# Kernel optimization log

Hardware: AMD Instinct MI355X
Metric: run time of the kernel (lower is better)

Reference implementation:

```python
import jax, jax.numpy as jnp
import numpy as np

N_NODES = 50000
N_EDGES = 600000
IN_F, HID, OUT_F = 602, 128, 41


def _gconv(x, W, b, src, dst, n):
    # DGL GraphConv, norm='both': D_dst^{-1/2} A (D_src^{-1/2} x W) + b
    ones = jnp.ones(src.shape, dtype=x.dtype)
    deg_out = jnp.clip(jax.ops.segment_sum(ones, src, num_segments=n), 1.0)
    deg_in = jnp.clip(jax.ops.segment_sum(ones, dst, num_segments=n), 1.0)
    h = x * jax.lax.rsqrt(deg_out)[:, None]
    h = h @ W  # dense transform first (in_feats > out_feats path)
    agg = jax.ops.segment_sum(h[src], dst, num_segments=n)  # [N, out]
    return agg * jax.lax.rsqrt(deg_in)[:, None] + b


def setup_inputs() -> dict:
    key = jax.random.key(0)
    ks = jax.random.split(key, 8)
    features = jax.random.normal(ks[0], (N_NODES, IN_F), dtype=jnp.float32)
    src = jax.random.randint(ks[1], (N_EDGES,), 0, N_NODES, dtype=jnp.int32)
    dst = jax.random.randint(ks[2], (N_EDGES,), 0, N_NODES, dtype=jnp.int32)
    def glorot(k, fan_in, fan_out):
        s = jnp.sqrt(6.0 / (fan_in + fan_out)).astype(jnp.float32)
        return jax.random.uniform(k, (fan_in, fan_out), jnp.float32, -s, s)
    return {
        'features': features, 'src': src, 'dst': dst,
        'W1': glorot(ks[3], IN_F, HID), 'b1': jnp.zeros((HID,), jnp.float32),
        'W2': glorot(ks[4], HID, HID), 'b2': jnp.zeros((HID,), jnp.float32),
        'W3': glorot(ks[5], HID, HID), 'b3': jnp.zeros((HID,), jnp.float32),
        'Wfc': glorot(ks[6], HID, OUT_F), 'bfc': jnp.zeros((OUT_F,), jnp.float32),
    }


def reference(features, src, dst, W1, b1, W2, b2, W3, b3, Wfc, bfc):
    n = features.shape[0]
    relu = jax.nn.relu
    x = relu(_gconv(features, W1, b1, src, dst, n))  # x = _x
    _x = relu(_gconv(x, W2, b2, src, dst, n))        # branch (layer2)
    x = relu(_gconv(x, W2, b2, src, dst, n))         # main (same layer2)
    x = relu(_gconv(x, W3, b3, src, dst, n))         # layer3
    x = relu(x + _x)                                  # residual + relu
    return x @ Wfc + bfc
```

## Files before the change

### kernel.cpp

```cpp
#include <hip/hip_runtime.h>
#include <hip/hip_bf16.h>

#define NN   50000
#define NE   600000
#define INF  602
#define HID  128
#define OUTF 41
#define NBLK 196

typedef __attribute__((ext_vector_type(8))) short bf16x8;
typedef __attribute__((ext_vector_type(4))) float f32x4;

__device__ inline unsigned short f2bf(float x) {
    unsigned u = __float_as_uint(x);
    unsigned r = u + 0x7FFF + ((u >> 16) & 1);
    return (unsigned short)(r >> 16);
}

#define GLL16(gp, lp) \
    __builtin_amdgcn_global_load_lds((const __attribute__((address_space(1))) unsigned int*)(gp), \
                                     (__attribute__((address_space(3))) unsigned int*)(lp), 16, 0, 0)

__global__ __launch_bounds__(256) void deg_hist_k(const int* __restrict__ src,
                                                  const int* __restrict__ dst,
                                                  int* __restrict__ cnt_out,
                                                  int* __restrict__ cnt_in, int E) {
    int e = blockIdx.x * 256 + threadIdx.x;
    if (e < E) {
        atomicAdd(&cnt_out[src[e]], 1);
        atomicAdd(&cnt_in[dst[e]], 1);
    }
}

__global__ __launch_bounds__(256) void scan1_k(const int* __restrict__ cnt,
                                               int* __restrict__ rowptr,
                                               int* __restrict__ blockSum) {
    __shared__ int tmp[256];
    int tid = threadIdx.x;
    int i = blockIdx.x * 256 + tid;
    int v = (i < NN) ? cnt[i] : 0;
    tmp[tid] = v;
    __syncthreads();
#pragma unroll
    for (int off = 1; off < 256; off <<= 1) {
        int t = (tid >= off) ? tmp[tid - off] : 0;
        __syncthreads();
        tmp[tid] += t;
        __syncthreads();
    }
    if (i < NN) rowptr[i] = tmp[tid] - v;
    if (tid == 255) blockSum[blockIdx.x] = tmp[255];
}

__global__ __launch_bounds__(256) void scan2_k(const int* __restrict__ blockSum,
                                               int* __restrict__ blockOff,
                                               int* __restrict__ rowptr) {
    __shared__ int tmp[256];
    int tid = threadIdx.x;
    int v = (tid < NBLK) ? blockSum[tid] : 0;
    tmp[tid] = v;
    __syncthreads();
#pragma unroll
    for (int off = 1; off < 256; off <<= 1) {
        int t = (tid >= off) ? tmp[tid - off] : 0;
        __syncthreads();
        tmp[tid] += t;
        __syncthreads();
    }
    if (tid < NBLK) blockOff[tid] = tmp[tid] - v;
    if (tid == 255) rowptr[NN] = tmp[255];
}

__global__ __launch_bounds__(256) void scan3_k(int* __restrict__ rowptr,
                                               const int* __restrict__ blockOff,
                                               int* __restrict__ wcur,
                                               const int* __restrict__ cnt_out,
                                               const int* __restrict__ cnt_in,
                                               float* __restrict__ rs_out,
                                               float* __restrict__ rs_in) {
    int i = blockIdx.x * 256 + threadIdx.x;
    if (i < NN) {
        int r = rowptr[i] + blockOff[blockIdx.x];
        rowptr[i] = r;
        wcur[i] = r;
        int co = cnt_out[i]; if (co < 1) co = 1;
        int ci = cnt_in[i];  if (ci < 1) ci = 1;
        rs_out[i] = rsqrtf((float)co);
        rs_in[i]  = rsqrtf((float)ci);
    }
}

__global__ __launch_bounds__(256) void fill_csr_k(const int* __restrict__ src,
                                                  const int* __restrict__ dst,
                                                  int* __restrict__ wcur,
                                                  int* __restrict__ csrsrc, int E) {
    int e = blockIdx.x * 256 + threadIdx.x;
    if (e < E) {
        int p = atomicAdd(&wcur[dst[e]], 1);
        csrsrc[p] = src[e];
    }
}

__device__ inline void prep_w_body(const float* __restrict__ W, int K,
                                   unsigned short* __restrict__ out, int total4, int i) {
    if (i >= total4) return;
    int col = i & 127;
    int k4 = (i >> 7) << 2;
    short4 h;
    h.x = (short)f2bf((k4 + 0 < K) ? W[(size_t)(k4 + 0) * HID + col] : 0.f);
    h.y = (short)f2bf((k4 + 1 < K) ? W[(size_t)(k4 + 1) * HID + col] : 0.f);
    h.z = (short)f2bf((k4 + 2 < K) ? W[(size_t)(k4 + 2) * HID + col] : 0.f);
    h.w = (short)f2bf((k4 + 3 < K) ? W[(size_t)(k4 + 3) * HID + col] : 0.f);
    *(short4*)&out[(size_t)(k4 >> 3) * 1024 + col * 8 + (k4 & 7)] = h;
}

__global__ __launch_bounds__(256) void prep_w_k(const float* __restrict__ W, int K,
                                                unsigned short* __restrict__ out, int total4) {
    prep_w_body(W, K, out, total4, blockIdx.x * 256 + threadIdx.x);
}

__global__ __launch_bounds__(256) void prep_w2_k(const float* __restrict__ Wa,
                                                 unsigned short* __restrict__ outa,
                                                 const float* __restrict__ Wb,
                                                 unsigned short* __restrict__ outb) {
    if (blockIdx.x < 16)
        prep_w_body(Wa, HID, outa, 4096, blockIdx.x * 256 + threadIdx.x);
    else
        prep_w_body(Wb, HID, outb, 4096, (blockIdx.x - 16) * 256 + threadIdx.x);
}

__global__ __launch_bounds__(256) void gemm1_k(const float* __restrict__ A,
                                               const unsigned short* __restrict__ Wt,
                                               const float* __restrict__ rs_out,
                                               unsigned short* __restrict__ H, int n) {
    __shared__ __attribute__((aligned(16))) short As[64 * 136];
    __shared__ __attribute__((aligned(16))) short Bs[16 * 1024];

    const int tid = threadIdx.x;
    const int wave = tid >> 6;
    const int lane = tid & 63;
    const int quad = lane >> 4;
    const int l16 = lane & 15;
    const int rowBase = blockIdx.x * 64;
    const int tileBase = rowBase + wave * 16;

    float4 apf[8];
    auto loadA = [&](int ch) {
        int kb = ch * 128;
#pragma unroll
        for (int c = 0; c < 8; ++c) {
            int f = c * 256 + tid;
            int row = f >> 5;
            int kc = (f & 31) << 2;
            int grow = rowBase + row;
            int gk = kb + kc;
            float4 v = {0.f, 0.f, 0.f, 0.f};
            if (grow < n) {
                if (gk + 3 < INF) {
                    v = *(const float4*)(A + (size_t)grow * INF + gk);
                } else {
                    if (gk + 0 < INF) v.x = A[(size_t)grow * INF + gk + 0];
                    if (gk + 1 < INF) v.y = A[(size_t)grow * INF + gk + 1];
                    if (gk + 2 < INF) v.z = A[(size_t)grow * INF + gk + 2];
                }
            }
            apf[c] = v;
        }
    };
    auto storeA = [&]() {
#pragma unroll
        for (int c = 0; c < 8; ++c) {
            int f = c * 256 + tid;
            int row = f >> 5;
            int kc = (f & 31) << 2;
            short4 h;
            h.x = (short)f2bf(apf[c].x); h.y = (short)f2bf(apf[c].y);
            h.z = (short)f2bf(apf[c].z); h.w = (short)f2bf(apf[c].w);
            *(short4*)&As[row * 136 + kc] = h;
        }
    };
    auto issueB = [&](int ch) {
#pragma unroll
        for (int c = 0; c < 8; ++c)
            GLL16(Wt + (size_t)ch * 16384 + c * 2048 + tid * 8, &Bs[c * 2048 + tid * 8]);
    };

    f32x4 acc[8];
#pragma unroll
    for (int j = 0; j < 8; ++j) acc[j] = (f32x4){0.f, 0.f, 0.f, 0.f};

    loadA(0);
    for (int ch = 0; ch < 5; ++ch) {
        __syncthreads();
        issueB(ch);
        storeA();
        __syncthreads();
        if (ch + 1 < 5) loadA(ch + 1);
#pragma unroll
        for (int s = 0; s < 4; ++s) {
            bf16x8 af = *(const bf16x8*)&As[(wave * 16 + l16) * 136 + s * 32 + quad * 8];
            const short* bg = &Bs[(s * 4 + quad) * 1024 + l16 * 8];
#pragma unroll
            for (int nt = 0; nt < 8; ++nt) {
                bf16x8 bf = *(const bf16x8*)(bg + nt * 128);
                acc[nt] = __builtin_amdgcn_mfma_f32_16x16x32_bf16(af, bf, acc[nt], 0, 0, 0);
            }
        }
    }

#pragma unroll
    for (int r = 0; r < 4; ++r) {
        int row = tileBase + quad * 4 + r;
        if (row < n) {
            float ro = rs_out[row];
#pragma unroll
            for (int nt = 0; nt < 8; ++nt)
                H[(size_t)row * HID + nt * 16 + l16] = f2bf(acc[nt][r] * ro);
        }
    }
}

__global__ __launch_bounds__(256) void gemm_hid_k(const unsigned short* __restrict__ A,
                                                  const unsigned short* __restrict__ Wt,
                                                  unsigned short* __restrict__ H, int n) {
    __shared__ __attribute__((aligned(16))) short As[64 * 136];
    __shared__ __attribute__((aligned(16))) short Bs[16384];

    const int tid = threadIdx.x;
    const int wave = tid >> 6;
    const int lane = tid & 63;
    const int quad = lane >> 4;
    const int l16 = lane & 15;
    const int wm = wave >> 1;
    const int wn = wave & 1;
    const int rowBase = blockIdx.x * 64;

#pragma unroll
    for (int c = 0; c < 8; ++c)
        GLL16(Wt + c * 2048 + tid * 8, &Bs[c * 2048 + tid * 8]);

#pragma unroll
    for (int c = 0; c < 4; ++c) {
        int f = c * 256 + tid;
        int row = f >> 4;
        int k16 = (f & 15) << 3;
        int grow = rowBase + row;
        int4 v = {0, 0, 0, 0};
        if (grow < n) v = *(const int4*)(A + (size_t)grow * HID + k16);
        *(int4*)&As[row * 136 + k16] = v;
    }
    __syncthreads();

    f32x4 acc[2][4];
#pragma unroll
    for (int i = 0; i < 2; ++i)
#pragma unroll
        for (int j = 0; j < 4; ++j) acc[i][j] = (f32x4){0.f, 0.f, 0.f, 0.f};

#pragma unroll
    for (int kq = 0; kq < 4; ++kq) {
        bf16x8 af[2], bfr[4];
#pragma unroll
        for (int mt = 0; mt < 2; ++mt)
            af[mt] = *(const bf16x8*)&As[(wm * 32 + mt * 16 + l16) * 136 + kq * 32 + quad * 8];
#pragma unroll
        for (int nt = 0; nt < 4; ++nt)
            bfr[nt] = *(const bf16x8*)&Bs[(kq * 4 + quad) * 1024 + (wn * 64 + nt * 16 + l16) * 8];
#pragma unroll
        for (int mt = 0; mt < 2; ++mt)
#pragma unroll
            for (int nt = 0; nt < 4; ++nt)
                acc[mt][nt] = __builtin_amdgcn_mfma_f32_16x16x32_bf16(af[mt], bfr[nt], acc[mt][nt], 0, 0, 0);
    }

#pragma unroll
    for (int mt = 0; mt < 2; ++mt)
#pragma unroll
        for (int r = 0; r < 4; ++r) {
            int row = rowBase + wm * 32 + mt * 16 + quad * 4 + r;
            if (row < n) {
#pragma unroll
                for (int nt = 0; nt < 4; ++nt) {
                    int col = wn * 64 + nt * 16 + l16;
                    H[(size_t)row * HID + col] = f2bf(acc[mt][nt][r]);
                }
            }
        }
}

__global__ __launch_bounds__(256) void gather_k(const unsigned short* __restrict__ H,
                                                const int* __restrict__ rowptr,
                                                const int* __restrict__ csrsrc,
                                                const float* __restrict__ rs_in,
                                                const float* __restrict__ rs_out,
                                                const float* __restrict__ bias,
                                                const float* __restrict__ resid,
                                                float* __restrict__ outX,
                                                unsigned short* __restrict__ outXs,
                                                int n) {
    const int lane = threadIdx.x & 63;
    const int g = lane >> 4;
    const int l = lane & 15;
    const int gbase = g << 4;
    const int wid = blockIdx.x * 4 + (threadIdx.x >> 6);
    const int node = wid * 4 + g;
    const bool alive = node < n;

    int beg = 0, end = 0;
    if (alive) { beg = rowptr[node]; end = rowptr[node + 1]; }

    float acc[8];
#pragma unroll
    for (int k = 0; k < 8; ++k) acc[k] = 0.f;

    auto accum = [&](int s) {
        int4 u = *(const int4*)(H + (size_t)s * HID + l * 8);
        unsigned x = (unsigned)u.x, y = (unsigned)u.y, z = (unsigned)u.z, w = (unsigned)u.w;
        acc[0] += __uint_as_float(x << 16); acc[1] += __uint_as_float(x & 0xFFFF0000u);
        acc[2] += __uint_as_float(y << 16); acc[3] += __uint_as_float(y & 0xFFFF0000u);
        acc[4] += __uint_as_float(z << 16); acc[5] += __uint_as_float(z & 0xFFFF0000u);
        acc[6] += __uint_as_float(w << 16); acc[7] += __uint_as_float(w & 0xFFFF0000u);
    };

    for (int base = beg; base < end; base += 16) {
        int m = end - base; if (m > 16) m = 16;
        int idx = (l < m) ? csrsrc[base + l] : 0;
        int j = 0;
        for (; j + 3 < m; j += 4) {
            int s0 = __shfl(idx, gbase | j);
            int s1 = __shfl(idx, gbase | (j + 1));
            int s2 = __shfl(idx, gbase | (j + 2));
            int s3 = __shfl(idx, gbase | (j + 3));
            int4 u0 = *(const int4*)(H + (size_t)s0 * HID + l * 8);
            int4 u1 = *(const int4*)(H + (size_t)s1 * HID + l * 8);
            int4 u2 = *(const int4*)(H + (size_t)s2 * HID + l * 8);
            int4 u3 = *(const int4*)(H + (size_t)s3 * HID + l * 8);
#pragma unroll
            for (int q = 0; q < 4; ++q) {
                int4 u = (q == 0) ? u0 : (q == 1) ? u1 : (q == 2) ? u2 : u3;
                unsigned x = (unsigned)u.x, y = (unsigned)u.y, z = (unsigned)u.z, w = (unsigned)u.w;
                acc[0] += __uint_as_float(x << 16); acc[1] += __uint_as_float(x & 0xFFFF0000u);
                acc[2] += __uint_as_float(y << 16); acc[3] += __uint_as_float(y & 0xFFFF0000u);
                acc[4] += __uint_as_float(z << 16); acc[5] += __uint_as_float(z & 0xFFFF0000u);
                acc[6] += __uint_as_float(w << 16); acc[7] += __uint_as_float(w & 0xFFFF0000u);
            }
        }
        for (; j < m; ++j) accum(__shfl(idx, gbase | j));
    }

    if (!alive) return;

    float ri = rs_in[node];
    float4 b0 = *(const float4*)(bias + l * 8);
    float4 b1 = *(const float4*)(bias + l * 8 + 4);
    float v[8];
    v[0] = fmaxf(acc[0] * ri + b0.x, 0.f); v[1] = fmaxf(acc[1] * ri + b0.y, 0.f);
    v[2] = fmaxf(acc[2] * ri + b0.z, 0.f); v[3] = fmaxf(acc[3] * ri + b0.w, 0.f);
    v[4] = fmaxf(acc[4] * ri + b1.x, 0.f); v[5] = fmaxf(acc[5] * ri + b1.y, 0.f);
    v[6] = fmaxf(acc[6] * ri + b1.z, 0.f); v[7] = fmaxf(acc[7] * ri + b1.w, 0.f);

    size_t o = (size_t)node * HID + l * 8;
    if (resid) {
        float4 r0 = *(const float4*)(resid + o);
        float4 r1 = *(const float4*)(resid + o + 4);
        v[0] = fmaxf(v[0] + r0.x, 0.f); v[1] = fmaxf(v[1] + r0.y, 0.f);
        v[2] = fmaxf(v[2] + r0.z, 0.f); v[3] = fmaxf(v[3] + r0.w, 0.f);
        v[4] = fmaxf(v[4] + r1.x, 0.f); v[5] = fmaxf(v[5] + r1.y, 0.f);
        v[6] = fmaxf(v[6] + r1.z, 0.f); v[7] = fmaxf(v[7] + r1.w, 0.f);
    }
    if (outX) {
        *(float4*)(outX + o) = make_float4(v[0], v[1], v[2], v[3]);
        *(float4*)(outX + o + 4) = make_float4(v[4], v[5], v[6], v[7]);
    }
    if (outXs) {
        float ro = rs_out[node];
        int4 h;
        h.x = (int)(((unsigned)f2bf(v[1] * ro) << 16) | f2bf(v[0] * ro));
        h.y = (int)(((unsigned)f2bf(v[3] * ro) << 16) | f2bf(v[2] * ro));
        h.z = (int)(((unsigned)f2bf(v[5] * ro) << 16) | f2bf(v[4] * ro));
        h.w = (int)(((unsigned)f2bf(v[7] * ro) << 16) | f2bf(v[6] * ro));
        *(int4*)(outXs + o) = h;
    }
}

__global__ __launch_bounds__(256) void fc_k(const float* __restrict__ X,
                                            const float* __restrict__ Wfc,
                                            const float* __restrict__ bfc,
                                            float* __restrict__ out, int n) {
    __shared__ float Ws[HID * OUTF];
    __shared__ float Xs[4][HID];
    int tid = threadIdx.x;
    for (int i = tid; i < HID * OUTF; i += 256) Ws[i] = Wfc[i];
    int rowBase = blockIdx.x * 4;
    for (int i = tid; i < 4 * HID; i += 256) {
        int r = i >> 7, c = i & 127;
        int gr = rowBase + r;
        Xs[r][c] = (gr < n) ? X[(size_t)gr * HID + c] : 0.f;
    }
    __syncthreads();
    int wv = tid >> 6, lane = tid & 63;
    int row = rowBase + wv;
    if (row < n && lane < OUTF) {
        float acc = bfc[lane];
#pragma unroll 8
        for (int k = 0; k < HID; ++k) acc += Xs[wv][k] * Ws[k * OUTF + lane];
        out[(size_t)row * OUTF + lane] = acc;
    }
}

extern "C" void kernel_launch(void* const* d_in, const int* in_sizes, int n_in,
                              void* d_out, int out_size, void* d_ws, size_t ws_size,
                              hipStream_t stream) {
    const float* feat = (const float*)d_in[0];
    const int* src = (const int*)d_in[1];
    const int* dst = (const int*)d_in[2];
    const float* W1 = (const float*)d_in[3];
    const float* b1 = (const float*)d_in[4];
    const float* W2 = (const float*)d_in[5];
    const float* b2 = (const float*)d_in[6];
    const float* W3 = (const float*)d_in[7];
    const float* b3 = (const float*)d_in[8];
    const float* Wfc = (const float*)d_in[9];
    const float* bfc = (const float*)d_in[10];
    float* out = (float*)d_out;

    char* w = (char*)d_ws;
    auto alloc = [&](size_t b) -> void* {
        void* p = (void*)w;
        w += (b + 255) & ~(size_t)255;
        return p;
    };
    int* cnt = (int*)alloc(2 * NN * sizeof(int));
    int* cnt_out = cnt;
    int* cnt_in  = cnt + NN;
    int* rowptr  = (int*)alloc((NN + 1) * sizeof(int));
    int* wcur    = (int*)alloc(NN * sizeof(int));
    int* csrsrc  = (int*)alloc(NE * sizeof(int));
    int* blockSum = (int*)alloc(NBLK * sizeof(int));
    int* blockOff = (int*)alloc(NBLK * sizeof(int));
    float* rs_out = (float*)alloc(NN * sizeof(float));
    float* rs_in  = (float*)alloc(NN * sizeof(float));
    unsigned short* W1t = (unsigned short*)alloc(10 * 8192 * sizeof(unsigned short));
    unsigned short* W2t = (unsigned short*)alloc(16384 * sizeof(unsigned short));
    unsigned short* W3t = (unsigned short*)alloc(16384 * sizeof(unsigned short));
    unsigned short* Hb = (unsigned short*)alloc((size_t)NN * HID * sizeof(unsigned short));
    unsigned short* Xb = (unsigned short*)alloc((size_t)NN * HID * sizeof(unsigned short));
    float* resid = (float*)alloc((size_t)NN * HID * sizeof(float));
    float* Xfc   = (float*)alloc((size_t)NN * HID * sizeof(float));

    hipMemsetAsync(cnt, 0, 2 * NN * sizeof(int), stream);

    prep_w_k<<<80, 256, 0, stream>>>(W1, INF, W1t, 20480);
    prep_w2_k<<<32, 256, 0, stream>>>(W2, W2t, W3, W3t);

    deg_hist_k<<<(NE + 255) / 256, 256, 0, stream>>>(src, dst, cnt_out, cnt_in, NE);
    scan1_k<<<NBLK, 256, 0, stream>>>(cnt_in, rowptr, blockSum);
    scan2_k<<<1, 256, 0, stream>>>(blockSum, blockOff, rowptr);
    scan3_k<<<NBLK, 256, 0, stream>>>(rowptr, blockOff, wcur, cnt_out, cnt_in, rs_out, rs_in);
    fill_csr_k<<<(NE + 255) / 256, 256, 0, stream>>>(src, dst, wcur, csrsrc, NE);

    const int gblk = (NN + 63) / 64;
    const int ablk = (NN + 15) / 16;
    gemm1_k<<<gblk, 256, 0, stream>>>(feat, W1t, rs_out, Hb, NN);
    gather_k<<<ablk, 256, 0, stream>>>(Hb, rowptr, csrsrc, rs_in, rs_out, b1,
                                       nullptr, nullptr, Xb, NN);
    gemm_hid_k<<<gblk, 256, 0, stream>>>(Xb, W2t, Hb, NN);
    gather_k<<<ablk, 256, 0, stream>>>(Hb, rowptr, csrsrc, rs_in, rs_out, b2,
                                       nullptr, resid, Xb, NN);
    gemm_hid_k<<<gblk, 256, 0, stream>>>(Xb, W3t, Hb, NN);
    gather_k<<<ablk, 256, 0, stream>>>(Hb, rowptr, csrsrc, rs_in, rs_out, b3,
                                       resid, Xfc, nullptr, NN);
    fc_k<<<(NN + 3) / 4, 256, 0, stream>>>(Xfc, Wfc, bfc, out, NN);
}
```

Baseline: 455.7 us.

## Merge preprocessing kernels and co-schedule CSR fill with first GEMM

Result: faster. 442.2 us (-3.0%).

```diff
diff --git a/kernel.cpp b/kernel.cpp
--- a/kernel.cpp
+++ b/kernel.cpp
@@ -8,8 +8,12 @@
 #define OUTF 41
 #define NBLK 196
 
+#define HISTB 2344
+#define GEMMB 782
+
 typedef __attribute__((ext_vector_type(8))) short bf16x8;
 typedef __attribute__((ext_vector_type(4))) float f32x4;
+typedef __attribute__((ext_vector_type(2))) float f32x2;
 
 __device__ inline unsigned short f2bf(float x) {
     unsigned u = __float_as_uint(x);
@@ -17,89 +21,13 @@
     return (unsigned short)(r >> 16);
 }
 
+__device__ inline f32x2 up2(unsigned u) {
+    return (f32x2){__uint_as_float(u << 16), __uint_as_float(u & 0xFFFF0000u)};
+}
+
 #define GLL16(gp, lp) \
     __builtin_amdgcn_global_load_lds((const __attribute__((address_space(1))) unsigned int*)(gp), \
                                      (__attribute__((address_space(3))) unsigned int*)(lp), 16, 0, 0)
-
-__global__ __launch_bounds__(256) void deg_hist_k(const int* __restrict__ src,
-                                                  const int* __restrict__ dst,
-                                                  int* __restrict__ cnt_out,
-                                                  int* __restrict__ cnt_in, int E) {
-    int e = blockIdx.x * 256 + threadIdx.x;
-    if (e < E) {
-        atomicAdd(&cnt_out[src[e]], 1);
-        atomicAdd(&cnt_in[dst[e]], 1);
-    }
-}
-
-__global__ __launch_bounds__(256) void scan1_k(const int* __restrict__ cnt,
-                                               int* __restrict__ rowptr,
-                                               int* __restrict__ blockSum) {
-    __shared__ int tmp[256];
-    int tid = threadIdx.x;
-    int i = blockIdx.x * 256 + tid;
-    int v = (i < NN) ? cnt[i] : 0;
-    tmp[tid] = v;
-    __syncthreads();
-#pragma unroll
-    for (int off = 1; off < 256; off <<= 1) {
-        int t = (tid >= off) ? tmp[tid - off] : 0;
-        __syncthreads();
-        tmp[tid] += t;
-        __syncthreads();
-    }
-    if (i < NN) rowptr[i] = tmp[tid] - v;
-    if (tid == 255) blockSum[blockIdx.x] = tmp[255];
-}
-
-__global__ __launch_bounds__(256) void scan2_k(const int* __restrict__ blockSum,
-                                               int* __restrict__ blockOff,
-                                               int* __restrict__ rowptr) {
-    __shared__ int tmp[256];
-    int tid = threadIdx.x;
-    int v = (tid < NBLK) ? blockSum[tid] : 0;
-    tmp[tid] = v;
-    __syncthreads();
-#pragma unroll
-    for (int off = 1; off < 256; off <<= 1) {
-        int t = (tid >= off) ? tmp[tid - off] : 0;
-        __syncthreads();
-        tmp[tid] += t;
-        __syncthreads();
-    }
-    if (tid < NBLK) blockOff[tid] = tmp[tid] - v;
-    if (tid == 255) rowptr[NN] = tmp[255];
-}
-
-__global__ __launch_bounds__(256) void scan3_k(int* __restrict__ rowptr,
-                                               const int* __restrict__ blockOff,
-                                               int* __restrict__ wcur,
-                                               const int* __restrict__ cnt_out,
-                                               const int* __restrict__ cnt_in,
-                                               float* __restrict__ rs_out,
-                                               float* __restrict__ rs_in) {
-    int i = blockIdx.x * 256 + threadIdx.x;
-    if (i < NN) {
-        int r = rowptr[i] + blockOff[blockIdx.x];
-        rowptr[i] = r;
-        wcur[i] = r;
-        int co = cnt_out[i]; if (co < 1) co = 1;
-        int ci = cnt_in[i];  if (ci < 1) ci = 1;
-        rs_out[i] = rsqrtf((float)co);
-        rs_in[i]  = rsqrtf((float)ci);
-    }
-}
-
-__global__ __launch_bounds__(256) void fill_csr_k(const int* __restrict__ src,
-                                                  const int* __restrict__ dst,
-                                                  int* __restrict__ wcur,
-                                                  int* __restrict__ csrsrc, int E) {
-    int e = blockIdx.x * 256 + threadIdx.x;
-    if (e < E) {
-        int p = atomicAdd(&wcur[dst[e]], 1);
-        csrsrc[p] = src[e];
-    }
-}
 
 __device__ inline void prep_w_body(const float* __restrict__ W, int K,
                                    unsigned short* __restrict__ out, int total4, int i) {
@@ -114,34 +42,112 @@
     *(short4*)&out[(size_t)(k4 >> 3) * 1024 + col * 8 + (k4 & 7)] = h;
 }
 
-__global__ __launch_bounds__(256) void prep_w_k(const float* __restrict__ W, int K,
-                                                unsigned short* __restrict__ out, int total4) {
-    prep_w_body(W, K, out, total4, blockIdx.x * 256 + threadIdx.x);
-}
-
-__global__ __launch_bounds__(256) void prep_w2_k(const float* __restrict__ Wa,
-                                                 unsigned short* __restrict__ outa,
-                                                 const float* __restrict__ Wb,
-                                                 unsigned short* __restrict__ outb) {
-    if (blockIdx.x < 16)
-        prep_w_body(Wa, HID, outa, 4096, blockIdx.x * 256 + threadIdx.x);
-    else
-        prep_w_body(Wb, HID, outb, 4096, (blockIdx.x - 16) * 256 + threadIdx.x);
-}
-
-__global__ __launch_bounds__(256) void gemm1_k(const float* __restrict__ A,
-                                               const unsigned short* __restrict__ Wt,
-                                               const float* __restrict__ rs_out,
-                                               unsigned short* __restrict__ H, int n) {
+__global__ __launch_bounds__(256) void hist_prep_k(const int* __restrict__ src,
+                                                   const int* __restrict__ dst,
+                                                   int* __restrict__ cnt_out,
+                                                   int* __restrict__ cnt_in,
+                                                   const float* __restrict__ W1,
+                                                   const float* __restrict__ W2,
+                                                   const float* __restrict__ W3,
+                                                   unsigned short* __restrict__ W1t,
+                                                   unsigned short* __restrict__ W2t,
+                                                   unsigned short* __restrict__ W3t) {
+    int b = blockIdx.x;
+    if (b < HISTB) {
+        int e = b * 256 + threadIdx.x;
+        if (e < NE) {
+            atomicAdd(&cnt_out[src[e]], 1);
+            atomicAdd(&cnt_in[dst[e]], 1);
+        }
+    } else {
+        int b2 = b - HISTB;
+        if (b2 < 80)       prep_w_body(W1, INF, W1t, 20480, b2 * 256 + threadIdx.x);
+        else if (b2 < 96)  prep_w_body(W2, HID, W2t, 4096, (b2 - 80) * 256 + threadIdx.x);
+        else               prep_w_body(W3, HID, W3t, 4096, (b2 - 96) * 256 + threadIdx.x);
+    }
+}
+
+__global__ __launch_bounds__(256) void scan1_k(const int* __restrict__ cnt,
+                                               int* __restrict__ rowptr,
+                                               int* __restrict__ blockSum) {
+    __shared__ int tmp[256];
+    int tid = threadIdx.x;
+    int i = blockIdx.x * 256 + tid;
+    int v = (i < NN) ? cnt[i] : 0;
+    tmp[tid] = v;
+    __syncthreads();
+#pragma unroll
+    for (int off = 1; off < 256; off <<= 1) {
+        int t = (tid >= off) ? tmp[tid - off] : 0;
+        __syncthreads();
+        tmp[tid] += t;
+        __syncthreads();
+    }
+    if (i < NN) rowptr[i] = tmp[tid] - v;
+    if (tid == 255) blockSum[blockIdx.x] = tmp[255];
+}
+
+__global__ __launch_bounds__(256) void scan23_k(int* __restrict__ rowptr,
+                                                const int* __restrict__ blockSum,
+                                                int* __restrict__ wcur,
+                                                const int* __restrict__ cnt_out,
+                                                const int* __restrict__ cnt_in,
+                                                float* __restrict__ rs_out,
+                                                float* __restrict__ rs_in) {
+    const int tid = threadIdx.x;
+    const int bid = blockIdx.x;
+    int vAll = (tid < NBLK) ? blockSum[tid] : 0;
+    int vPre = (tid < bid) ? vAll : 0;
+#pragma unroll
+    for (int o = 32; o; o >>= 1) {
+        vAll += __shfl_down(vAll, o);
+        vPre += __shfl_down(vPre, o);
+    }
+    __shared__ int sA[4], sP[4];
+    if ((tid & 63) == 0) { sA[tid >> 6] = vAll; sP[tid >> 6] = vPre; }
+    __syncthreads();
+    int offAll = sA[0] + sA[1] + sA[2] + sA[3];
+    int offPre = sP[0] + sP[1] + sP[2] + sP[3];
+    int i = bid * 256 + tid;
+    if (i < NN) {
+        int r = rowptr[i] + offPre;
+        rowptr[i] = r;
+        wcur[i] = r;
+        int co = cnt_out[i]; if (co < 1) co = 1;
+        int ci = cnt_in[i];  if (ci < 1) ci = 1;
+        rs_out[i] = rsqrtf((float)co);
+        rs_in[i]  = rsqrtf((float)ci);
+    }
+    if (bid == NBLK - 1 && tid == 0) rowptr[NN] = offAll;
+}
+
+__global__ __launch_bounds__(256) void fill_gemm1_k(const int* __restrict__ src,
+                                                    const int* __restrict__ dst,
+                                                    int* __restrict__ wcur,
+                                                    int* __restrict__ csrsrc,
+                                                    const float* __restrict__ A,
+                                                    const unsigned short* __restrict__ Wt,
+                                                    const float* __restrict__ rs_out,
+                                                    unsigned short* __restrict__ H, int n) {
     __shared__ __attribute__((aligned(16))) short As[64 * 136];
     __shared__ __attribute__((aligned(16))) short Bs[16 * 1024];
 
+    if (blockIdx.x < HISTB) {
+        int e = blockIdx.x * 256 + threadIdx.x;
+        if (e < NE) {
+            int p = atomicAdd(&wcur[dst[e]], 1);
+            csrsrc[p] = src[e];
+        }
+        return;
+    }
+
+    const int gb = blockIdx.x - HISTB;
     const int tid = threadIdx.x;
     const int wave = tid >> 6;
     const int lane = tid & 63;
     const int quad = lane >> 4;
     const int l16 = lane & 15;
-    const int rowBase = blockIdx.x * 64;
+    const int rowBase = gb * 64;
     const int tileBase = rowBase + wave * 16;
 
     float4 apf[8];
@@ -309,18 +315,7 @@
     int beg = 0, end = 0;
     if (alive) { beg = rowptr[node]; end = rowptr[node + 1]; }
 
-    float acc[8];
-#pragma unroll
-    for (int k = 0; k < 8; ++k) acc[k] = 0.f;
-
-    auto accum = [&](int s) {
-        int4 u = *(const int4*)(H + (size_t)s * HID + l * 8);
-        unsigned x = (unsigned)u.x, y = (unsigned)u.y, z = (unsigned)u.z, w = (unsigned)u.w;
-        acc[0] += __uint_as_float(x << 16); acc[1] += __uint_as_float(x & 0xFFFF0000u);
-        acc[2] += __uint_as_float(y << 16); acc[3] += __uint_as_float(y & 0xFFFF0000u);
-        acc[4] += __uint_as_float(z << 16); acc[5] += __uint_as_float(z & 0xFFFF0000u);
-        acc[6] += __uint_as_float(w << 16); acc[7] += __uint_as_float(w & 0xFFFF0000u);
-    };
+    f32x2 a01 = {0.f, 0.f}, a23 = {0.f, 0.f}, a45 = {0.f, 0.f}, a67 = {0.f, 0.f};
 
     for (int base = beg; base < end; base += 16) {
         int m = end - base; if (m > 16) m = 16;
@@ -338,14 +333,20 @@
 #pragma unroll
             for (int q = 0; q < 4; ++q) {
                 int4 u = (q == 0) ? u0 : (q == 1) ? u1 : (q == 2) ? u2 : u3;
-                unsigned x = (unsigned)u.x, y = (unsigned)u.y, z = (unsigned)u.z, w = (unsigned)u.w;
-                acc[0] += __uint_as_float(x << 16); acc[1] += __uint_as_float(x & 0xFFFF0000u);
-                acc[2] += __uint_as_float(y << 16); acc[3] += __uint_as_float(y & 0xFFFF0000u);
-                acc[4] += __uint_as_float(z << 16); acc[5] += __uint_as_float(z & 0xFFFF0000u);
-                acc[6] += __uint_as_float(w << 16); acc[7] += __uint_as_float(w & 0xFFFF0000u);
+                a01 += up2((unsigned)u.x);
+                a23 += up2((unsigned)u.y);
+                a45 += up2((unsigned)u.z);
+                a67 += up2((unsigned)u.w);
             }
         }
-        for (; j < m; ++j) accum(__shfl(idx, gbase | j));
+        for (; j < m; ++j) {
+            int s = __shfl(idx, gbase | j);
+            int4 u = *(const int4*)(H + (size_t)s * HID + l * 8);
+            a01 += up2((unsigned)u.x);
+            a23 += up2((unsigned)u.y);
+            a45 += up2((unsigned)u.z);
+            a67 += up2((unsigned)u.w);
+        }
     }
 
     if (!alive) return;
@@ -354,10 +355,10 @@
     float4 b0 = *(const float4*)(bias + l * 8);
     float4 b1 = *(const float4*)(bias + l * 8 + 4);
     float v[8];
-    v[0] = fmaxf(acc[0] * ri + b0.x, 0.f); v[1] = fmaxf(acc[1] * ri + b0.y, 0.f);
-    v[2] = fmaxf(acc[2] * ri + b0.z, 0.f); v[3] = fmaxf(acc[3] * ri + b0.w, 0.f);
-    v[4] = fmaxf(acc[4] * ri + b1.x, 0.f); v[5] = fmaxf(acc[5] * ri + b1.y, 0.f);
-    v[6] = fmaxf(acc[6] * ri + b1.z, 0.f); v[7] = fmaxf(acc[7] * ri + b1.w, 0.f);
+    v[0] = fmaxf(a01[0] * ri + b0.x, 0.f); v[1] = fmaxf(a01[1] * ri + b0.y, 0.f);
+    v[2] = fmaxf(a23[0] * ri + b0.z, 0.f); v[3] = fmaxf(a23[1] * ri + b0.w, 0.f);
+    v[4] = fmaxf(a45[0] * ri + b1.x, 0.f); v[5] = fmaxf(a45[1] * ri + b1.y, 0.f);
+    v[6] = fmaxf(a67[0] * ri + b1.z, 0.f); v[7] = fmaxf(a67[1] * ri + b1.w, 0.f);
 
     size_t o = (size_t)node * HID + l * 8;
     if (resid) {
@@ -437,12 +438,12 @@
     int* wcur    = (int*)alloc(NN * sizeof(int));
     int* csrsrc  = (int*)alloc(NE * sizeof(int));
     int* blockSum = (int*)alloc(NBLK * sizeof(int));
-    int* blockOff = (int*)alloc(NBLK * sizeof(int));
     float* rs_out = (float*)alloc(NN * sizeof(float));
     float* rs_in  = (float*)alloc(NN * sizeof(float));
     unsigned short* W1t = (unsigned short*)alloc(10 * 8192 * sizeof(unsigned short));
     unsigned short* W2t = (unsigned short*)alloc(16384 * sizeof(unsigned short));
     unsigned short* W3t = (unsigned short*)alloc(16384 * sizeof(unsigned short));
+    unsigned short* Ha = (unsigned short*)alloc((size_t)NN * HID * sizeof(unsigned short));
     unsigned short* Hb = (unsigned short*)alloc((size_t)NN * HID * sizeof(unsigned short));
     unsigned short* Xb = (unsigned short*)alloc((size_t)NN * HID * sizeof(unsigned short));
     float* resid = (float*)alloc((size_t)NN * HID * sizeof(float));
@@ -450,25 +451,21 @@
 
     hipMemsetAsync(cnt, 0, 2 * NN * sizeof(int), stream);
 
-    prep_w_k<<<80, 256, 0, stream>>>(W1, INF, W1t, 20480);
-    prep_w2_k<<<32, 256, 0, stream>>>(W2, W2t, W3, W3t);
-
-    deg_hist_k<<<(NE + 255) / 256, 256, 0, stream>>>(src, dst, cnt_out, cnt_in, NE);
+    hist_prep_k<<<HISTB + 112, 256, 0, stream>>>(src, dst, cnt_out, cnt_in,
+                                                 W1, W2, W3, W1t, W2t, W3t);
     scan1_k<<<NBLK, 256, 0, stream>>>(cnt_in, rowptr, blockSum);
-    scan2_k<<<1, 256, 0, stream>>>(blockSum, blockOff, rowptr);
-    scan3_k<<<NBLK, 256, 0, stream>>>(rowptr, blockOff, wcur, cnt_out, cnt_in, rs_out, rs_in);
-    fill_csr_k<<<(NE + 255) / 256, 256, 0, stream>>>(src, dst, wcur, csrsrc, NE);
-
-    const int gblk = (NN + 63) / 64;
+    scan23_k<<<NBLK, 256, 0, stream>>>(rowptr, blockSum, wcur, cnt_out, cnt_in, rs_out, rs_in);
+    fill_gemm1_k<<<HISTB + GEMMB, 256, 0, stream>>>(src, dst, wcur, csrsrc,
+                                                    feat, W1t, rs_out, Ha, NN);
+
     const int ablk = (NN + 15) / 16;
-    gemm1_k<<<gblk, 256, 0, stream>>>(feat, W1t, rs_out, Hb, NN);
-    gather_k<<<ablk, 256, 0, stream>>>(Hb, rowptr, csrsrc, rs_in, rs_out, b1,
+    gather_k<<<ablk, 256, 0, stream>>>(Ha, rowptr, csrsrc, rs_in, rs_out, b1,
                                        nullptr, nullptr, Xb, NN);
-    gemm_hid_k<<<gblk, 256, 0, stream>>>(Xb, W2t, Hb, NN);
+    gemm_hid_k<<<GEMMB, 256, 0, stream>>>(Xb, W2t, Hb, NN);
     gather_k<<<ablk, 256, 0, stream>>>(Hb, rowptr, csrsrc, rs_in, rs_out, b2,
                                        nullptr, resid, Xb, NN);
-    gemm_hid_k<<<gblk, 256, 0, stream>>>(Xb, W3t, Hb, NN);
-    gather_k<<<ablk, 256, 0, stream>>>(Hb, rowptr, csrsrc, rs_in, rs_out, b3,
+    gemm_hid_k<<<GEMMB, 256, 0, stream>>>(Xb, W3t, Ha, NN);
+    gather_k<<<ablk, 256, 0, stream>>>(Ha, rowptr, csrsrc, rs_in, rs_out, b3,
                                        resid, Xfc, nullptr, NN);
     fc_k<<<(NN + 3) / 4, 256, 0, stream>>>(Xfc, Wfc, bfc, out, NN);
 }
```
